# Performance work log

Measured on AMD Instinct MI355X. Metric: run time of the kernel, lower is better.

The kernel has to match this reference:

```python
import jax, jax.numpy as jnp
import numpy as np

H = 64  # hidden size
I = 1   # input size


def setup_inputs() -> dict:
    key = jax.random.key(0)
    ks = jax.random.split(key, 7)
    B, T = 4096, 512
    s_ih = 1.0 / np.sqrt(H)
    x = jax.random.normal(ks[0], (B, T, I), dtype=jnp.float32)
    # torch nn.GRU params: weight_ih [3H, I], weight_hh [3H, H], biases [3H]
    W_ih = jax.random.uniform(ks[1], (3 * H, I), minval=-s_ih, maxval=s_ih, dtype=jnp.float32)
    W_hh = jax.random.uniform(ks[2], (3 * H, H), minval=-s_ih, maxval=s_ih, dtype=jnp.float32)
    b_ih = jax.random.uniform(ks[3], (3 * H,), minval=-s_ih, maxval=s_ih, dtype=jnp.float32)
    b_hh = jax.random.uniform(ks[4], (3 * H,), minval=-s_ih, maxval=s_ih, dtype=jnp.float32)
    # final Linear(64, 1)
    W_out = jax.random.uniform(ks[5], (1, H), minval=-s_ih, maxval=s_ih, dtype=jnp.float32)
    b_out = jax.random.uniform(ks[6], (1,), minval=-s_ih, maxval=s_ih, dtype=jnp.float32)
    return {"x": x, "W_ih": W_ih, "W_hh": W_hh, "b_ih": b_ih, "b_hh": b_hh,
            "W_out": W_out, "b_out": b_out}


def _gru_last_hidden(x, W_ih, W_hh, b_ih, b_hh):
    B, T, _ = x.shape
    # precompute input projections for all timesteps: [B, T, 3H]
    xp = jnp.einsum('bti,gi->btg', x, W_ih) + b_ih
    xp = jnp.swapaxes(xp, 0, 1)  # [T, B, 3H]
    Whr, Whz, Whn = W_hh[:H], W_hh[H:2 * H], W_hh[2 * H:]
    bhr, bhz, bhn = b_hh[:H], b_hh[H:2 * H], b_hh[2 * H:]

    def step(h, xt):
        xr, xz, xn = xt[:, :H], xt[:, H:2 * H], xt[:, 2 * H:]
        r = jax.nn.sigmoid(xr + h @ Whr.T + bhr)
        z = jax.nn.sigmoid(xz + h @ Whz.T + bhz)
        n = jnp.tanh(xn + r * (h @ Whn.T + bhn))
        h_new = (1.0 - z) * n + z * h
        return h_new, None

    h0 = jnp.zeros((B, H), dtype=x.dtype)
    h_last, _ = jax.lax.scan(step, h0, xp)
    return h_last


def reference(x, W_ih, W_hh, b_ih, b_hh, W_out, b_out):
    h_last = _gru_last_hidden(x, W_ih, W_hh, b_ih, b_hh)
    return h_last @ W_out.T + b_out  # [B, 1]
```

## Files before the change

### kernel.cpp

```cpp
#include <hip/hip_runtime.h>
#include <stdint.h>

#define TT 512
#define BT 16

typedef float    f32x4 __attribute__((ext_vector_type(4)));
typedef float    f32x2 __attribute__((ext_vector_type(2)));
typedef short    s16x8 __attribute__((ext_vector_type(8)));
typedef _Float16 f16x8 __attribute__((ext_vector_type(8)));

#define MFMA_F16(A, B, C) \
    __builtin_amdgcn_mfma_f32_16x16x32_f16( \
        __builtin_bit_cast(f16x8, (A)), (B), (C), 0, 0, 0)

#define LOG2E  1.442695040888963f
#define LOG2E2 2.885390081777927f

static __device__ __forceinline__ unsigned bits(float v) {
    union { float f; unsigned u; } x; x.f = v; return x.u;
}

__global__ __launch_bounds__(256) void gru_scan_kernel(
    const float* __restrict__ x,
    const float* __restrict__ Wih,
    const float* __restrict__ Whh,
    const float* __restrict__ bih,
    const float* __restrict__ bhh,
    const float* __restrict__ Wout,
    const float* __restrict__ bout,
    float* __restrict__ out)
{
    __shared__ __align__(16) float xs2[TT * BT];
    __shared__ __align__(16) short hbuf[2][2][64][8];
    __shared__ float outp[4][BT];

    const int tid  = threadIdx.x;
    const int w    = tid >> 6;
    const int L    = tid & 63;
    const int n16  = L & 15;
    const int quad = L >> 4;
    const int q    = w * 16 + n16;
    const int b0   = blockIdx.x * BT;

    #pragma unroll
    for (int k = 0; k < 8; ++k) {
        int idx = tid + k * 256;
        int row = idx >> 7;
        int t4  = idx & 127;
        f32x4 v = *(const f32x4*)(x + (size_t)(b0 + row) * TT + t4 * 4);
        #pragma unroll
        for (int i = 0; i < 4; ++i)
            xs2[(t4 * 4 + i) * BT + row] = v[i];
    }
    if (tid < 256) {
        f32x4* hb = (f32x4*)hbuf;
        f32x4 zv = {0.f, 0.f, 0.f, 0.f};
        hb[tid] = zv;
    }

    const float wr2   = -LOG2E  * Wih[q];
    const float wz2   = -LOG2E  * Wih[64 + q];
    const float wn2   =  LOG2E2 * Wih[128 + q];
    const float bR2   = -LOG2E  * (bih[q]      + bhh[q]);
    const float bZ2   = -LOG2E  * (bih[64 + q] + bhh[64 + q]);
    const float bN2   =  LOG2E2 * bhh[128 + q];
    const float bihn2 =  LOG2E2 * bih[128 + q];
    const float wo    = Wout[q];

    f16x8 Bf[3][2];
    #pragma unroll
    for (int g = 0; g < 3; ++g) {
        const float sg = (g == 2) ? LOG2E2 : -LOG2E;
        #pragma unroll
        for (int c = 0; c < 2; ++c) {
            const float* p = Whh + ((g * 64 + q) * 64 + c * 32 + quad * 8);
            #pragma unroll
            for (int j = 0; j < 8; ++j)
                Bf[g][c][j] = (_Float16)(p[j] * sg);
        }
    }

    float hD[4] = {0.f, 0.f, 0.f, 0.f};

    const int cw = q >> 5;
    const int qd = (q & 31) >> 3;
    const int jw = q & 7;

    const s16x8* hbv = (const s16x8*)hbuf;

    auto step = [&](int cur, int t) {
        __syncthreads();

        s16x8 A0 = hbv[cur * 128 +  0 + L];
        s16x8 A1 = hbv[cur * 128 + 64 + L];
        f32x4 xq = *(const f32x4*)(xs2 + t * BT + quad * 4);

        f32x4 aR = {bR2, bR2, bR2, bR2};
        f32x4 aZ = {bZ2, bZ2, bZ2, bZ2};
        f32x4 aN = {bN2, bN2, bN2, bN2};

        aR = MFMA_F16(A0, Bf[0][0], aR);
        aZ = MFMA_F16(A0, Bf[1][0], aZ);
        aN = MFMA_F16(A0, Bf[2][0], aN);
        aR = MFMA_F16(A1, Bf[0][1], aR);
        aZ = MFMA_F16(A1, Bf[1][1], aZ);
        aN = MFMA_F16(A1, Bf[2][1], aN);

        const int nxt = cur ^ 1;
        short* wh = (short*)hbuf + nxt * 1024 + cw * 512 + qd * 128 + jw;

        #pragma unroll
        for (int p = 0; p < 4; p += 2) {
            f32x2 aRp = {aR[p], aR[p + 1]};
            f32x2 aZp = {aZ[p], aZ[p + 1]};
            f32x2 aNp = {aN[p], aN[p + 1]};
            f32x2 xv  = {xq[p], xq[p + 1]};
            f32x2 hp  = {hD[p], hD[p + 1]};

            f32x2 ar = xv * wr2 + aRp;
            f32x2 az = xv * wz2 + aZp;
            f32x2 Er = {__builtin_amdgcn_exp2f(ar[0]), __builtin_amdgcn_exp2f(ar[1])};
            f32x2 Ez = {__builtin_amdgcn_exp2f(az[0]), __builtin_amdgcn_exp2f(az[1])};
            f32x2 DR = Er + 1.0f;
            f32x2 DZ = Ez + 1.0f;
            f32x2 P  = DR * DZ;
            f32x2 ip = {__builtin_amdgcn_rcpf(P[0]), __builtin_amdgcn_rcpf(P[1])};
            f32x2 r  = ip * DZ;
            f32x2 z  = ip * DR;
            f32x2 xn = xv * wn2 + bihn2;
            f32x2 an = r * aNp + xn;
            f32x2 En = {__builtin_amdgcn_exp2f(an[0]), __builtin_amdgcn_exp2f(an[1])};
            f32x2 DN = En + 1.0f;
            f32x2 rn = {__builtin_amdgcn_rcpf(DN[0]), __builtin_amdgcn_rcpf(DN[1])};
            f32x2 n  = rn * -2.0f + 1.0f;
            f32x2 hn = z * (hp - n) + n;

            hD[p] = hn[0]; hD[p + 1] = hn[1];

            const int m0 = quad * 4 + p;
            wh[m0 * 8]       = __builtin_bit_cast(short, (_Float16)hn[0]);
            wh[(m0 + 1) * 8] = __builtin_bit_cast(short, (_Float16)hn[1]);
        }
    };

    for (int t = 0; t < TT; t += 2) {
        step(0, t);
        step(1, t + 1);
    }

    float p[4];
    #pragma unroll
    for (int reg = 0; reg < 4; ++reg) p[reg] = hD[reg] * wo;
    #pragma unroll
    for (int mask = 1; mask <= 8; mask <<= 1) {
        #pragma unroll
        for (int reg = 0; reg < 4; ++reg)
            p[reg] += __shfl_xor(p[reg], mask, 64);
    }
    if (n16 == 0) {
        #pragma unroll
        for (int reg = 0; reg < 4; ++reg)
            outp[w][quad * 4 + reg] = p[reg];
    }
    __syncthreads();
    if (tid < BT) {
        out[b0 + tid] = outp[0][tid] + outp[1][tid] + outp[2][tid] + outp[3][tid] + bout[0];
    }
}

extern "C" void kernel_launch(void* const* d_in, const int* in_sizes, int n_in,
                              void* d_out, int out_size, void* d_ws, size_t ws_size,
                              hipStream_t stream) {
    (void)in_sizes; (void)n_in; (void)d_ws; (void)ws_size; (void)out_size;
    const float* x    = (const float*)d_in[0];
    const float* Wih  = (const float*)d_in[1];
    const float* Whh  = (const float*)d_in[2];
    const float* bih  = (const float*)d_in[3];
    const float* bhh  = (const float*)d_in[4];
    const float* Wout = (const float*)d_in[5];
    const float* bout = (const float*)d_in[6];
    float* out = (float*)d_out;

    gru_scan_kernel<<<dim3(4096 / BT), dim3(256), 0, stream>>>(
        x, Wih, Whh, bih, bhh, Wout, bout, out);
}
```

Measured before the change: 212.5 us.

## Double wavefronts per block, splitting gate elementwise rows across wave pairs

Launches 512 threads per block instead of 256. Each pair of waves computes the same MFMA tile redundantly, and each wave then handles only 2 of the 4 output rows in the sigmoid/tanh elementwise phase. This halves the per-wave transcendental work on the serial timestep critical path. The gate math is also reordered so each row uses two reciprocals, and the final reduction now sums over 8 waves. The cost is duplicated MFMA work, more LDS write contention, and a larger barrier across 8 waves every step.

```diff
diff --git a/kernel.cpp b/kernel.cpp
--- a/kernel.cpp
+++ b/kernel.cpp
@@ -16,11 +16,7 @@
 #define LOG2E  1.442695040888963f
 #define LOG2E2 2.885390081777927f
 
-static __device__ __forceinline__ unsigned bits(float v) {
-    union { float f; unsigned u; } x; x.f = v; return x.u;
-}
-
-__global__ __launch_bounds__(256) void gru_scan_kernel(
+__global__ __launch_bounds__(512) void gru_scan_kernel(
     const float* __restrict__ x,
     const float* __restrict__ Wih,
     const float* __restrict__ Whh,
@@ -32,19 +28,21 @@
 {
     __shared__ __align__(16) float xs2[TT * BT];
     __shared__ __align__(16) short hbuf[2][2][64][8];
-    __shared__ float outp[4][BT];
+    __shared__ float outp[8][BT];
 
     const int tid  = threadIdx.x;
-    const int w    = tid >> 6;
+    const int wv   = tid >> 6;
     const int L    = tid & 63;
     const int n16  = L & 15;
     const int quad = L >> 4;
-    const int q    = w * 16 + n16;
+    const int colw = wv & 3;
+    const int q    = colw * 16 + n16;
+    const int rb   = (wv >> 2) * 2;
     const int b0   = blockIdx.x * BT;
 
     #pragma unroll
-    for (int k = 0; k < 8; ++k) {
-        int idx = tid + k * 256;
+    for (int k = 0; k < 4; ++k) {
+        int idx = tid + k * 512;
         int row = idx >> 7;
         int t4  = idx & 127;
         f32x4 v = *(const f32x4*)(x + (size_t)(b0 + row) * TT + t4 * 4);
@@ -67,6 +65,10 @@
     const float bihn2 =  LOG2E2 * bih[128 + q];
     const float wo    = Wout[q];
 
+    const f32x4 bR4 = {bR2, bR2, bR2, bR2};
+    const f32x4 bZ4 = {bZ2, bZ2, bZ2, bZ2};
+    const f32x4 bN4 = {bN2, bN2, bN2, bN2};
+
     f16x8 Bf[3][2];
     #pragma unroll
     for (int g = 0; g < 3; ++g) {
@@ -80,11 +82,12 @@
         }
     }
 
-    float hD[4] = {0.f, 0.f, 0.f, 0.f};
+    float hD[2] = {0.f, 0.f};
 
     const int cw = q >> 5;
     const int qd = (q & 31) >> 3;
     const int jw = q & 7;
+    const int m0 = quad * 4 + rb;
 
     const s16x8* hbv = (const s16x8*)hbuf;
 
@@ -93,53 +96,45 @@
 
         s16x8 A0 = hbv[cur * 128 +  0 + L];
         s16x8 A1 = hbv[cur * 128 + 64 + L];
-        f32x4 xq = *(const f32x4*)(xs2 + t * BT + quad * 4);
+        f32x2 xv2 = *(const f32x2*)(xs2 + t * BT + m0);
 
-        f32x4 aR = {bR2, bR2, bR2, bR2};
-        f32x4 aZ = {bZ2, bZ2, bZ2, bZ2};
-        f32x4 aN = {bN2, bN2, bN2, bN2};
-
-        aR = MFMA_F16(A0, Bf[0][0], aR);
-        aZ = MFMA_F16(A0, Bf[1][0], aZ);
-        aN = MFMA_F16(A0, Bf[2][0], aN);
-        aR = MFMA_F16(A1, Bf[0][1], aR);
-        aZ = MFMA_F16(A1, Bf[1][1], aZ);
-        aN = MFMA_F16(A1, Bf[2][1], aN);
+        f32x4 aR = MFMA_F16(A0, Bf[0][0], bR4);
+        aR       = MFMA_F16(A1, Bf[0][1], aR);
+        f32x4 aN = MFMA_F16(A0, Bf[2][0], bN4);
+        aN       = MFMA_F16(A1, Bf[2][1], aN);
+        f32x4 aZ = MFMA_F16(A0, Bf[1][0], bZ4);
+        aZ       = MFMA_F16(A1, Bf[1][1], aZ);
 
         const int nxt = cur ^ 1;
         short* wh = (short*)hbuf + nxt * 1024 + cw * 512 + qd * 128 + jw;
 
         #pragma unroll
-        for (int p = 0; p < 4; p += 2) {
-            f32x2 aRp = {aR[p], aR[p + 1]};
-            f32x2 aZp = {aZ[p], aZ[p + 1]};
-            f32x2 aNp = {aN[p], aN[p + 1]};
-            f32x2 xv  = {xq[p], xq[p + 1]};
-            f32x2 hp  = {hD[p], hD[p + 1]};
+        for (int p = 0; p < 2; ++p) {
+            const int reg = rb + p;
+            float aRp = aR[reg], aZp = aZ[reg], aNp = aN[reg];
+            float xv  = xv2[p];
+            float hp  = hD[p];
 
-            f32x2 ar = xv * wr2 + aRp;
-            f32x2 az = xv * wz2 + aZp;
-            f32x2 Er = {__builtin_amdgcn_exp2f(ar[0]), __builtin_amdgcn_exp2f(ar[1])};
-            f32x2 Ez = {__builtin_amdgcn_exp2f(az[0]), __builtin_amdgcn_exp2f(az[1])};
-            f32x2 DR = Er + 1.0f;
-            f32x2 DZ = Ez + 1.0f;
-            f32x2 P  = DR * DZ;
-            f32x2 ip = {__builtin_amdgcn_rcpf(P[0]), __builtin_amdgcn_rcpf(P[1])};
-            f32x2 r  = ip * DZ;
-            f32x2 z  = ip * DR;
-            f32x2 xn = xv * wn2 + bihn2;
-            f32x2 an = r * aNp + xn;
-            f32x2 En = {__builtin_amdgcn_exp2f(an[0]), __builtin_amdgcn_exp2f(an[1])};
-            f32x2 DN = En + 1.0f;
-            f32x2 rn = {__builtin_amdgcn_rcpf(DN[0]), __builtin_amdgcn_rcpf(DN[1])};
-            f32x2 n  = rn * -2.0f + 1.0f;
-            f32x2 hn = z * (hp - n) + n;
+            float ar = __builtin_fmaf(xv, wr2, aRp);
+            float Er = __builtin_amdgcn_exp2f(ar);
+            float DR = Er + 1.0f;
+            float r  = __builtin_amdgcn_rcpf(DR);
+            float az = __builtin_fmaf(xv, wz2, aZp);
+            float Ez = __builtin_amdgcn_exp2f(az);
+            float DZ = Ez + 1.0f;
+            float xn = __builtin_fmaf(xv, wn2, bihn2);
+            float an = __builtin_fmaf(r, aNp, xn);
+            float En = __builtin_amdgcn_exp2f(an);
+            float DN = En + 1.0f;
+            float PD = DZ * DN;
+            float iq = __builtin_amdgcn_rcpf(PD);
+            float z  = iq * DN;
+            float rn = iq * DZ;
+            float n  = __builtin_fmaf(-2.0f, rn, 1.0f);
+            float hn = __builtin_fmaf(z, hp - n, n);
 
-            hD[p] = hn[0]; hD[p + 1] = hn[1];
-
-            const int m0 = quad * 4 + p;
-            wh[m0 * 8]       = __builtin_bit_cast(short, (_Float16)hn[0]);
-            wh[(m0 + 1) * 8] = __builtin_bit_cast(short, (_Float16)hn[1]);
+            hD[p] = hn;
+            wh[(m0 + p) * 8] = __builtin_bit_cast(short, (_Float16)hn);
         }
     };
 
@@ -148,23 +143,25 @@
         step(1, t + 1);
     }
 
-    float p[4];
-    #pragma unroll
-    for (int reg = 0; reg < 4; ++reg) p[reg] = hD[reg] * wo;
+    if (tid < 128) ((float*)outp)[tid] = 0.0f;
+    float p0 = hD[0] * wo;
+    float p1 = hD[1] * wo;
     #pragma unroll
     for (int mask = 1; mask <= 8; mask <<= 1) {
-        #pragma unroll
-        for (int reg = 0; reg < 4; ++reg)
-            p[reg] += __shfl_xor(p[reg], mask, 64);
+        p0 += __shfl_xor(p0, mask, 64);
+        p1 += __shfl_xor(p1, mask, 64);
     }
+    __syncthreads();
     if (n16 == 0) {
-        #pragma unroll
-        for (int reg = 0; reg < 4; ++reg)
-            outp[w][quad * 4 + reg] = p[reg];
+        outp[wv][m0]     = p0;
+        outp[wv][m0 + 1] = p1;
     }
     __syncthreads();
     if (tid < BT) {
-        out[b0 + tid] = outp[0][tid] + outp[1][tid] + outp[2][tid] + outp[3][tid] + bout[0];
+        float s = bout[0];
+        #pragma unroll
+        for (int wsum = 0; wsum < 8; ++wsum) s += outp[wsum][tid];
+        out[b0 + tid] = s;
     }
 }
 
@@ -181,6 +178,6 @@
     const float* bout = (const float*)d_in[6];
     float* out = (float*)d_out;
 
-    gru_scan_kernel<<<dim3(4096 / BT), dim3(256), 0, stream>>>(
+    gru_scan_kernel<<<dim3(4096 / BT), dim3(512), 0, stream>>>(
         x, Wih, Whh, bih, bhh, Wout, bout, out);
 }
```

New measurement: 251.5 us. 1.18x slower.

## Replace transcendental intrinsics with packed polynomial exp2/rcp and swizzle hidden-state LDS layout

Applied to the files above, without the earlier changes.

Replaces the hardware exp2 and rcp intrinsics with software versions built from packed-friendly FMA: a magic-number polynomial exp2 and a bit-trick reciprocal refined by Newton iterations. It also rewrites the gate algebra so one combined reciprocal covers both z and the tanh denominator. The hidden-state LDS buffer gets a permuted, XOR-swizzled write/read layout to reduce bank conflicts, and the MFMA issue order is reshuffled. The aim is to move work off the transcendental unit and onto packed FMA along the serial per-step critical path. In exchange each transcendental costs more instructions and the approximations may lose some accuracy.

```diff
diff --git a/kernel.cpp b/kernel.cpp
--- a/kernel.cpp
+++ b/kernel.cpp
@@ -15,9 +15,34 @@
 
 #define LOG2E  1.442695040888963f
 #define LOG2E2 2.885390081777927f
+#define MAGIC  12582912.0f
 
 static __device__ __forceinline__ unsigned bits(float v) {
     union { float f; unsigned u; } x; x.f = v; return x.u;
+}
+static __device__ __forceinline__ float fbits(unsigned u) {
+    union { unsigned u; float f; } x; x.u = u; return x.f;
+}
+
+static __device__ __forceinline__ f32x2 exp2_pk(f32x2 a) {
+    f32x2 r0 = a + MAGIC;
+    f32x2 fi = r0 - MAGIC;
+    f32x2 f  = a - fi;
+    f32x2 p  = f * 0.00961813f + 0.05550411f;
+    p = p * f + 0.24022651f;
+    p = p * f + 0.69314718f;
+    p = p * f + 1.0f;
+    unsigned e0 = (bits(r0[0]) << 23) + bits(p[0]);
+    unsigned e1 = (bits(r0[1]) << 23) + bits(p[1]);
+    f32x2 E = {fbits(e0), fbits(e1)};
+    return E;
+}
+
+static __device__ __forceinline__ f32x2 rcp_pk(f32x2 x) {
+    f32x2 y = {fbits(0x7EF311C3u - bits(x[0])), fbits(0x7EF311C3u - bits(x[1]))};
+    y = y * (2.0f - x * y);
+    y = y * (2.0f - x * y);
+    return y;
 }
 
 __global__ __launch_bounds__(256) void gru_scan_kernel(
@@ -31,7 +56,7 @@
     float* __restrict__ out)
 {
     __shared__ __align__(16) float xs2[TT * BT];
-    __shared__ __align__(16) short hbuf[2][2][64][8];
+    __shared__ __align__(16) short hbuf[2][1024];
     __shared__ float outp[4][BT];
 
     const int tid  = threadIdx.x;
@@ -52,7 +77,7 @@
         for (int i = 0; i < 4; ++i)
             xs2[(t4 * 4 + i) * BT + row] = v[i];
     }
-    if (tid < 256) {
+    {
         f32x4* hb = (f32x4*)hbuf;
         f32x4 zv = {0.f, 0.f, 0.f, 0.f};
         hb[tid] = zv;
@@ -67,6 +92,10 @@
     const float bihn2 =  LOG2E2 * bih[128 + q];
     const float wo    = Wout[q];
 
+    const f32x4 bR4 = {bR2, bR2, bR2, bR2};
+    const f32x4 bZ4 = {bZ2, bZ2, bZ2, bZ2};
+    const f32x4 bN4 = {bN2, bN2, bN2, bN2};
+
     f16x8 Bf[3][2];
     #pragma unroll
     for (int g = 0; g < 3; ++g) {
@@ -82,32 +111,33 @@
 
     float hD[4] = {0.f, 0.f, 0.f, 0.f};
 
-    const int cw = q >> 5;
-    const int qd = (q & 31) >> 3;
-    const int jw = q & 7;
+    const int kg   = q >> 3;
+    const int sxor = (kg & 1) * 4;
+    int waddr[4];
+    #pragma unroll
+    for (int r = 0; r < 4; ++r)
+        waddr[r] = (kg * 16 + ((r * 4 + quad) ^ sxor)) * 8 + (q & 7);
+
+    const int permx = ((n16 & 3) * 4 + (n16 >> 2)) ^ ((quad & 1) * 4);
+    const int rslot = quad * 16 + permx;
 
     const s16x8* hbv = (const s16x8*)hbuf;
 
     auto step = [&](int cur, int t) {
         __syncthreads();
 
-        s16x8 A0 = hbv[cur * 128 +  0 + L];
-        s16x8 A1 = hbv[cur * 128 + 64 + L];
+        s16x8 A0 = hbv[cur * 128 +  0 + rslot];
+        s16x8 A1 = hbv[cur * 128 + 64 + rslot];
         f32x4 xq = *(const f32x4*)(xs2 + t * BT + quad * 4);
 
-        f32x4 aR = {bR2, bR2, bR2, bR2};
-        f32x4 aZ = {bZ2, bZ2, bZ2, bZ2};
-        f32x4 aN = {bN2, bN2, bN2, bN2};
-
-        aR = MFMA_F16(A0, Bf[0][0], aR);
-        aZ = MFMA_F16(A0, Bf[1][0], aZ);
-        aN = MFMA_F16(A0, Bf[2][0], aN);
-        aR = MFMA_F16(A1, Bf[0][1], aR);
-        aZ = MFMA_F16(A1, Bf[1][1], aZ);
-        aN = MFMA_F16(A1, Bf[2][1], aN);
-
-        const int nxt = cur ^ 1;
-        short* wh = (short*)hbuf + nxt * 1024 + cw * 512 + qd * 128 + jw;
+        f32x4 aR = MFMA_F16(A0, Bf[0][0], bR4);
+        aR       = MFMA_F16(A1, Bf[0][1], aR);
+        f32x4 aN = MFMA_F16(A0, Bf[2][0], bN4);
+        aN       = MFMA_F16(A1, Bf[2][1], aN);
+        f32x4 aZ = MFMA_F16(A0, Bf[1][0], bZ4);
+        aZ       = MFMA_F16(A1, Bf[1][1], aZ);
+
+        short* wh = (short*)hbuf + (cur ^ 1) * 1024;
 
         #pragma unroll
         for (int p = 0; p < 4; p += 2) {
@@ -119,27 +149,26 @@
 
             f32x2 ar = xv * wr2 + aRp;
             f32x2 az = xv * wz2 + aZp;
-            f32x2 Er = {__builtin_amdgcn_exp2f(ar[0]), __builtin_amdgcn_exp2f(ar[1])};
-            f32x2 Ez = {__builtin_amdgcn_exp2f(az[0]), __builtin_amdgcn_exp2f(az[1])};
+            f32x2 xn = xv * wn2 + bihn2;
+
+            f32x2 Er = exp2_pk(ar);
+            f32x2 Ez = exp2_pk(az);
             f32x2 DR = Er + 1.0f;
             f32x2 DZ = Ez + 1.0f;
-            f32x2 P  = DR * DZ;
-            f32x2 ip = {__builtin_amdgcn_rcpf(P[0]), __builtin_amdgcn_rcpf(P[1])};
-            f32x2 r  = ip * DZ;
-            f32x2 z  = ip * DR;
-            f32x2 xn = xv * wn2 + bihn2;
+            f32x2 r  = rcp_pk(DR);
             f32x2 an = r * aNp + xn;
-            f32x2 En = {__builtin_amdgcn_exp2f(an[0]), __builtin_amdgcn_exp2f(an[1])};
+            f32x2 En = exp2_pk(an);
             f32x2 DN = En + 1.0f;
-            f32x2 rn = {__builtin_amdgcn_rcpf(DN[0]), __builtin_amdgcn_rcpf(DN[1])};
-            f32x2 n  = rn * -2.0f + 1.0f;
-            f32x2 hn = z * (hp - n) + n;
+            f32x2 P  = DZ * DN;
+            f32x2 iq = rcp_pk(P);
+            f32x2 s2 = 2.0f - 2.0f * DZ;
+            f32x2 tt = (hp - 1.0f) * DN + s2;
+            f32x2 hn = iq * tt + 1.0f;
 
             hD[p] = hn[0]; hD[p + 1] = hn[1];
 
-            const int m0 = quad * 4 + p;
-            wh[m0 * 8]       = __builtin_bit_cast(short, (_Float16)hn[0]);
-            wh[(m0 + 1) * 8] = __builtin_bit_cast(short, (_Float16)hn[1]);
+            wh[waddr[p]]     = __builtin_bit_cast(short, (_Float16)hn[0]);
+            wh[waddr[p + 1]] = __builtin_bit_cast(short, (_Float16)hn[1]);
         }
     };
 
```

Result: slower. 264.5 us (+24.5%).
